# Optimization experiments

Hardware: AMD Instinct MI355X
Metric: run time of the kernel (lower is better)

Reference implementation:

```python
import jax, jax.numpy as jnp
import numpy as np

NUM_HEADS = 16


def rotate_half(x):
    half = x.shape[-1] // 2
    return jnp.concatenate((-x[..., half:], x[..., :half]), axis=-1)


def rope_tables(seq_len, head_dim, dtype=jnp.float32):
    inv_freq = 1.0 / (10000.0 ** (jnp.arange(0, head_dim, 2, dtype=jnp.float32) / head_dim))
    t = jnp.arange(seq_len, dtype=jnp.float32)
    freqs = jnp.outer(t, inv_freq)                 # [S, hd/2]
    emb = jnp.concatenate((freqs, freqs), axis=-1)  # [S, hd]
    return jnp.cos(emb).astype(dtype), jnp.sin(emb).astype(dtype)


def setup_inputs() -> dict:
    key = jax.random.key(0)
    k1, k2, k3 = jax.random.split(key, 3)
    B, S, D = 2, 2048, 1024
    x = jax.random.normal(k1, (B, S, D), dtype=jnp.float32)
    # causal lower-triangular mask, broadcast over batch/heads
    mask = jnp.tril(jnp.ones((S, S), dtype=bool))[None, None, :, :]
    w_qkv = jax.random.normal(k2, (3 * D, D), dtype=jnp.float32) * (D ** -0.5)
    w_out = jax.random.normal(k3, (D, D), dtype=jnp.float32) * (D ** -0.5)
    return {"x": x, "mask": mask, "w_qkv": w_qkv, "w_out": w_out}


def reference(x, mask, w_qkv, w_out):
    B, S, D = x.shape
    H = NUM_HEADS
    hd = D // H
    scale = hd ** -0.5

    qkv = jnp.einsum('bsd,ed->bse', x, w_qkv)          # [B, S, 3D]
    q, k, v = jnp.split(qkv, 3, axis=-1)

    def split(t):
        return t.reshape(B, S, H, hd).transpose(0, 2, 1, 3)  # [B, H, S, hd]

    q, k, v = split(q), split(k), split(v)

    cos, sin = rope_tables(S, hd, x.dtype)             # [S, hd]
    cos = cos[None, None]
    sin = sin[None, None]
    q = q * cos + rotate_half(q) * sin
    k = k * cos + rotate_half(k) * sin

    attn = jnp.einsum('bhqd,bhkd->bhqk', q, k) * scale  # [B, H, S, S]
    attn = jnp.where(mask, attn, jnp.float32(-jnp.inf).astype(attn.dtype))
    attn = jax.nn.softmax(attn, axis=-1)
    out = jnp.einsum('bhqk,bhkd->bhqd', attn, v)        # [B, H, S, hd]
    out = out.transpose(0, 2, 1, 3).reshape(B, S, D)
    return jnp.einsum('bsd,ed->bse', out, w_out)
```

## Files before the change

### kernel.cpp

```cpp
#include <hip/hip_runtime.h>
#include <hip/hip_bf16.h>

typedef __attribute__((ext_vector_type(8))) __bf16 bf16x8;
typedef __attribute__((ext_vector_type(4))) __bf16 bf16x4;
typedef __attribute__((ext_vector_type(2))) __bf16 bf16x2;
typedef __attribute__((ext_vector_type(4))) float f32x4;
typedef __attribute__((ext_vector_type(16))) float f32x16;

#define SEQ 2048
#define NH 16
#define HD 64
#define DMODEL 1024
#define BATCH 2
#define MTOT 4096
#define NSLOT 72

#if __has_builtin(__builtin_amdgcn_exp2f)
#define EXP2(x) __builtin_amdgcn_exp2f(x)
#else
#define EXP2(x) exp2f(x)
#endif
#define MFMA32(a, b, c) __builtin_amdgcn_mfma_f32_32x32x16_bf16(a, b, c, 0, 0, 0)

__device__ __forceinline__ void gl_lds16(const void* g, void* l) {
    __builtin_amdgcn_global_load_lds(
        (const __attribute__((address_space(1))) void*)(uintptr_t)g,
        (__attribute__((address_space(3))) void*)(uintptr_t)l,
        16, 0, 0);
}

__device__ __forceinline__ unsigned pk2(float x, float y) {
    union { bf16x2 h; unsigned u; } c;
    c.h = bf16x2{ (__bf16)x, (__bf16)y };
    return c.u;
}

#define TILE_SYNC(N) do {                                           \
    asm volatile("s_waitcnt vmcnt(" #N ")" ::: "memory");           \
    __builtin_amdgcn_s_barrier();                                   \
    __builtin_amdgcn_sched_barrier(0);                              \
} while (0)

__constant__ int4 FITEM[80] = {
    {31,0,16,68},{31,16,32,69},{31,32,48,70},{31,48,64,71},
    {23,0,16,37},{23,16,32,38},{23,32,48,39},
    {15,0,16,14},{15,16,32,15},
    {30,15,31,65},{30,46,62,67},
    {22,30,46,36},
    {7,0,16,-1},
    {29,0,15,60},{29,15,30,61},{29,30,45,62},{29,45,60,63},
    {30,0,15,64},{30,31,46,66},
    {22,0,15,34},{22,15,30,35},
    {21,14,29,32},{21,29,44,33},
    {28,14,29,57},{28,43,58,59},
    {14,0,15,12},{14,15,30,13},
    {27,0,14,52},{27,14,28,53},{27,28,42,54},{27,42,56,55},
    {28,0,14,56},{28,29,43,58},
    {20,0,14,28},{20,14,28,29},{20,28,42,30},
    {21,0,14,31},
    {26,13,27,49},{26,40,54,51},
    {19,26,40,27},
    {13,0,14,10},{13,14,28,11},
    {6,0,14,-1},
    {25,0,13,44},{25,13,26,45},{25,26,39,46},{25,39,52,47},
    {26,0,13,48},{26,27,40,50},
    {24,12,25,41},{24,37,50,43},
    {19,0,13,25},{19,13,26,26},
    {18,12,25,23},{18,25,38,24},
    {12,0,13,8},{12,13,26,9},
    {24,0,12,40},{24,25,37,42},
    {17,0,12,19},{17,12,24,20},{17,24,36,21},
    {18,0,12,22},
    {16,22,34,18},
    {11,0,12,6},{11,12,24,7},
    {5,0,12,-1},
    {16,0,11,16},{16,11,22,17},
    {10,0,11,4},{10,11,22,5},
    {9,0,10,2},{9,10,20,3},
    {4,0,10,-1},
    {8,0,9,0},{8,9,18,1},
    {3,0,8,-1},{2,0,6,-1},{1,0,4,-1},{0,0,2,-1}
};

__global__ __launch_bounds__(256) void cast3(const float4* __restrict__ x,
                                             const float4* __restrict__ wq,
                                             const float4* __restrict__ wo,
                                             __bf16* __restrict__ xb,
                                             __bf16* __restrict__ wqb,
                                             __bf16* __restrict__ wob) {
    const int NX  = 1024 * 1024;
    const int NWQ = 768 * 1024;
    const int NTOT = NX + NWQ + 256 * 1024;
    int i = blockIdx.x * 256 + threadIdx.x;
    if (i >= NTOT) return;
    float4 v; __bf16* dst; int j;
    if (i < NX)            { j = i;            v = x[j];  dst = xb;  }
    else if (i < NX + NWQ) { j = i - NX;       v = wq[j]; dst = wqb; }
    else                   { j = i - NX - NWQ; v = wo[j]; dst = wob; }
    bf16x4 o = { (__bf16)v.x, (__bf16)v.y, (__bf16)v.z, (__bf16)v.w };
    *(bf16x4*)(dst + (size_t)j * 4) = o;
}

__global__ __launch_bounds__(256) void gemm_qkv(const __bf16* __restrict__ A,
                                                const __bf16* __restrict__ Bt,
                                                __bf16* __restrict__ Qp,
                                                char* __restrict__ K2,
                                                char* __restrict__ V2) {
    const int K = 1024;
    __shared__ __align__(16) char lds[3 * 16384];
    const int tid = threadIdx.x, lane = tid & 63, wave = tid >> 6;
    const int lrow = lane & 15, quad = lane >> 4;
    const int bx = blockIdx.x, by = blockIdx.y;
    const int m0 = by * 128, n0 = bx * 128;
    const int wm = wave >> 1, wn = wave & 1;

    const __bf16* ap[2]; int aof[2];
    const __bf16* bp[2]; int bof[2];
#pragma unroll
    for (int i = 0; i < 2; ++i) {
        int r0 = i * 64 + wave * 16;
        int row = r0 + (lane >> 2);
        ap[i] = A + (size_t)(m0 + row) * K + (lane & 3) * 8;
        aof[i] = r0 * 64;
        bp[i] = Bt + (size_t)(n0 + row) * K + (lane & 3) * 8;
        bof[i] = 8192 + r0 * 64;
    }
    int arow[4], brow[4];
#pragma unroll
    for (int i = 0; i < 4; ++i) {
        arow[i] = wm * 64 + i * 16 + lrow;
        brow[i] = wn * 64 + i * 16 + lrow;
    }

    f32x4 z = {0.f, 0.f, 0.f, 0.f};
    f32x4 acc[4][4];
#pragma unroll
    for (int i = 0; i < 4; ++i)
#pragma unroll
        for (int j = 0; j < 4; ++j) acc[i][j] = z;

    auto STAGE = [&](char* base, int k0) {
#pragma unroll
        for (int i = 0; i < 2; ++i) gl_lds16(ap[i] + k0, base + aof[i]);
#pragma unroll
        for (int i = 0; i < 2; ++i) gl_lds16(bp[i] + k0, base + bof[i]);
    };
    auto COMPUTE = [&](const char* base) {
        bf16x8 af[4], bfr[4];
#pragma unroll
        for (int i = 0; i < 4; ++i)
            af[i] = *(const bf16x8*)(base + arow[i] * 64 + quad * 16);
#pragma unroll
        for (int i = 0; i < 4; ++i)
            bfr[i] = *(const bf16x8*)(base + 8192 + brow[i] * 64 + quad * 16);
        __builtin_amdgcn_s_setprio(1);
#pragma unroll
        for (int i = 0; i < 4; ++i)
#pragma unroll
            for (int j = 0; j < 4; ++j)
                acc[i][j] = __builtin_amdgcn_mfma_f32_16x16x32_bf16(
                    af[i], bfr[j], acc[i][j], 0, 0, 0);
        __builtin_amdgcn_s_setprio(0);
    };

    STAGE(lds, 0);
    STAGE(lds + 16384, 32);
    TILE_SYNC(4);
    for (int t = 0; t < 30; ++t) {
        STAGE(lds + ((t + 2) % 3) * 16384, (t + 2) * 32);
        COMPUTE(lds + (t % 3) * 16384);
        TILE_SYNC(4);
    }
    COMPUTE(lds + 0 * 16384);
    TILE_SYNC(0);
    COMPUTE(lds + 1 * 16384);

    const int nt = bx;
    const int sec = nt >> 3;
    const int b = m0 >> 11;
    const int s0b = m0 & (SEQ - 1);
    const int h = (nt & 7) * 2 + wn;
    const int bh = b * NH + h;

    if (sec < 2) {
        const float scale = sec ? 1.0f : 0.18033688011112042f;
        char* Kb = K2 + (size_t)bh * 262144;
        float invf0 = 0.15915494309189535f *
                      exp2f(-(float)lrow * 0.4152410118609203f);
        float invf1 = invf0 * 0.01f;
#pragma unroll
        for (int i = 0; i < 4; ++i) {
            int srow0 = s0b + wm * 64 + i * 16 + quad * 4;
#pragma unroll
            for (int j = 0; j < 2; ++j) {
                float invf = j ? invf1 : invf0;
                int hdlo = j * 16 + lrow;
#pragma unroll
                for (int r = 0; r < 4; ++r) {
                    int s = srow0 + r;
                    float rev = (float)s * invf;
                    float fr = rev - floorf(rev);
                    float sn = __builtin_amdgcn_sinf(fr);
                    float cs = __builtin_amdgcn_cosf(fr);
                    float lo = acc[i][j][r], hi = acc[i][j + 2][r];
                    float olo = (lo * cs - hi * sn) * scale;
                    float ohi = (hi * cs + lo * sn) * scale;
                    if (sec == 0) {
                        size_t base = ((size_t)bh * SEQ + s) * HD + hdlo;
                        Qp[base] = (__bf16)olo;
                        Qp[base + 32] = (__bf16)ohi;
                    } else {
                        char* kt = Kb + (s >> 5) * 4096 + (s & 31) * 16 +
                                   ((lrow >> 3) & 1) * 512 + (lrow & 7) * 2;
                        *(__bf16*)(kt + j * 1024) = (__bf16)olo;
                        *(__bf16*)(kt + (j + 2) * 1024) = (__bf16)ohi;
                    }
                }
            }
        }
    } else {
        char* Vb = V2 + (size_t)bh * 262144;
#pragma unroll
        for (int i = 0; i < 4; ++i) {
            int srow0 = s0b + wm * 64 + i * 16 + quad * 4;
            int kb = srow0 >> 4, ko = srow0 & 15;
            int slot0 = ((ko >> 2) & 1) * 8 + (ko >> 3) * 4;
#pragma unroll
            for (int j = 0; j < 4; ++j) {
                int ch = j * 16 + lrow;
                bf16x4 wv = { (__bf16)acc[i][j][0], (__bf16)acc[i][j][1],
                              (__bf16)acc[i][j][2], (__bf16)acc[i][j][3] };
                *(bf16x4*)(Vb + kb * 2048 + ch * 32 + slot0 * 2) = wv;
            }
        }
    }
}

__global__ __launch_bounds__(256) void gemm_bt(const __bf16* __restrict__ A,
                                               const __bf16* __restrict__ Bt,
                                               float* __restrict__ Cf,
                                               int M, int N, int K) {
    __shared__ __bf16 sA[2][128 * 64];
    __shared__ __bf16 sB[2][128 * 64];
    const int tid = threadIdx.x, lane = tid & 63, wave = tid >> 6;
    const int lrow = lane & 15, quad = lane >> 4;

    int lin = blockIdx.y * 8 + blockIdx.x;
    lin = (lin & 7) * 32 + (lin >> 3);
    const int bx = lin & 7, by = lin >> 3;
    const int m0 = by * 128, n0 = bx * 128;
    const int wm = wave >> 1, wn = wave & 1;

    const __bf16* ap[4]; const __bf16* bp[4]; int ldso[4];
#pragma unroll
    for (int i = 0; i < 4; ++i) {
        int r0 = i * 32 + wave * 8;
        int row = r0 + (lane >> 3);
        int cg = (lane & 7) ^ (row & 7);
        ap[i] = A + (size_t)(m0 + row) * K + cg * 8;
        bp[i] = Bt + (size_t)(n0 + row) * K + cg * 8;
        ldso[i] = r0 * 128;
    }
    int arow[4], brow[4];
#pragma unroll
    for (int i = 0; i < 4; ++i) {
        arow[i] = wm * 64 + i * 16 + lrow;
        brow[i] = wn * 64 + i * 16 + lrow;
    }

    f32x4 z = {0.f, 0.f, 0.f, 0.f};
    f32x4 acc[4][4];
#pragma unroll
    for (int i = 0; i < 4; ++i)
#pragma unroll
        for (int j = 0; j < 4; ++j) acc[i][j] = z;

    char* sA0 = (char*)sA[0]; char* sA1 = (char*)sA[1];
    char* sB0 = (char*)sB[0]; char* sB1 = (char*)sB[1];

    auto STAGE = [&](char* dA, char* dB, int k0) {
#pragma unroll
        for (int i = 0; i < 4; ++i) gl_lds16(ap[i] + k0, dA + ldso[i]);
#pragma unroll
        for (int i = 0; i < 4; ++i) gl_lds16(bp[i] + k0, dB + ldso[i]);
    };
    auto COMPUTE = [&](const char* sAb, const char* sBb) {
#pragma unroll
        for (int ks = 0; ks < 2; ++ks) {
            bf16x8 af[4], bfr[4];
#pragma unroll
            for (int i = 0; i < 4; ++i)
                af[i] = *(const bf16x8*)(sAb + arow[i] * 128 +
                                         (((ks * 4 + quad) ^ (arow[i] & 7)) << 4));
#pragma unroll
            for (int i = 0; i < 4; ++i)
                bfr[i] = *(const bf16x8*)(sBb + brow[i] * 128 +
                                          (((ks * 4 + quad) ^ (brow[i] & 7)) << 4));
#pragma unroll
            for (int i = 0; i < 4; ++i)
#pragma unroll
                for (int j = 0; j < 4; ++j)
                    acc[i][j] = __builtin_amdgcn_mfma_f32_16x16x32_bf16(
                        af[i], bfr[j], acc[i][j], 0, 0, 0);
        }
    };

    STAGE(sA0, sB0, 0);
    __syncthreads();
    for (int k0 = 0; k0 < K; k0 += 128) {
        if (k0 + 64 < K) STAGE(sA1, sB1, k0 + 64);
        COMPUTE(sA0, sB0);
        __syncthreads();
        if (k0 + 128 < K) STAGE(sA0, sB0, k0 + 128);
        COMPUTE(sA1, sB1);
        __syncthreads();
    }
#pragma unroll
    for (int i = 0; i < 4; ++i)
#pragma unroll
        for (int j = 0; j < 4; ++j)
#pragma unroll
            for (int r = 0; r < 4; ++r) {
                int row = m0 + wm * 64 + i * 16 + quad * 4 + r;
                int col = n0 + wn * 64 + j * 16 + lrow;
                Cf[(size_t)row * N + col] = acc[i][j][r];
            }
}

__global__ __launch_bounds__(64) void flash_attn(const __bf16* __restrict__ Qp,
                                                 const char* __restrict__ K2,
                                                 const char* __restrict__ V2,
                                                 __bf16* __restrict__ Aout,
                                                 __bf16* __restrict__ Opart,
                                                 float* __restrict__ Lpart) {
    const int lane = threadIdx.x;
    const int ql = lane & 31, half = lane >> 5;
    const int lin = blockIdx.x;
    const int xcd = lin & 7;
    const int j = lin >> 3;
    const int item = j % 80;
    const int bgroup = j / 80;
    const int bh = bgroup * 8 + xcd;
    const int4 it = FITEM[item];
    const int s = it.x, t0 = it.y, t1 = it.z, slot = it.w;
    const int b = bh >> 4, hh = bh & 15;

    const __bf16* qb = Qp + ((size_t)bh * SEQ + s * 64 + ql) * HD + half * 8;
    bf16x8 qf0[4], qf1[4];
#pragma unroll
    for (int kc = 0; kc < 4; ++kc) {
        qf0[kc] = *(const bf16x8*)(qb + kc * 16);
        qf1[kc] = *(const bf16x8*)(qb + 32 * HD + kc * 16);
    }
    const char* Kb = K2 + (size_t)bh * 262144 + half * 512 + ql * 16;
    const char* Vb = V2 + (size_t)bh * 262144 + ql * 32 + half * 16;

    f32x16 zz = {0.f};
    f32x16 oA0 = zz, oA1 = zz, oB0 = zz, oB1 = zz;
    float lA = 0.f, lB = 0.f;
    const int dA = 2 * s, dB = 2 * s + 1;
    const int thr = ql - 4 * half;

    auto STEP = [&](int t, const bf16x8* kf, bf16x8* kn) {
        bf16x8 vf[2][2];
#pragma unroll
        for (int lo = 0; lo < 2; ++lo) {
            const char* vp = Vb + (t * 2 + lo) * 2048;
            vf[lo][0] = *(const bf16x8*)(vp);
            vf[lo][1] = *(const bf16x8*)(vp + 1024);
        }
        if (t + 1 < t1) {
            const char* kt = Kb + (t + 1) * 4096;
#pragma unroll
            for (int kc = 0; kc < 4; ++kc)
                kn[kc] = *(const bf16x8*)(kt + kc * 1024);
        }
        const bool do0 = (t != dB);
        f32x16 st0 = zz, st1 = zz;
        if (do0) {
#pragma unroll
            for (int kc = 0; kc < 4; ++kc)
                st0 = MFMA32(kf[kc], qf0[kc], st0);
        }
#pragma unroll
        for (int kc = 0; kc < 4; ++kc)
            st1 = MFMA32(kf[kc], qf1[kc], st1);

        if (do0) {
#pragma unroll
            for (int i = 0; i < 16; ++i) st0[i] = EXP2(st0[i]);
            if (t == dA) {
#pragma unroll
                for (int g = 0; g < 4; ++g)
#pragma unroll
                    for (int tt = 0; tt < 4; ++tt)
                        if (8 * g + tt > thr) st0[g * 4 + tt] = 0.f;
            }
#pragma unroll
            for (int i = 0; i < 16; ++i) lA += st0[i];
        }
#pragma unroll
        for (int i = 0; i < 16; ++i) st1[i] = EXP2(st1[i]);
        if (t == dB) {
#pragma unroll
            for (int g = 0; g < 4; ++g)
#pragma unroll
                for (int tt = 0; tt < 4; ++tt)
                    if (8 * g + tt > thr) st1[g * 4 + tt] = 0.f;
        }
#pragma unroll
        for (int i = 0; i < 16; ++i) lB += st1[i];

#pragma unroll
        for (int lo = 0; lo < 2; ++lo) {
            if (do0) {
                union { unsigned u[4]; bf16x8 v; } p0;
#pragma unroll
                for (int d = 0; d < 4; ++d)
                    p0.u[d] = pk2(st0[lo * 8 + 2 * d], st0[lo * 8 + 2 * d + 1]);
                oA0 = MFMA32(vf[lo][0], p0.v, oA0);
                oA1 = MFMA32(vf[lo][1], p0.v, oA1);
            }
            union { unsigned u[4]; bf16x8 v; } p1;
#pragma unroll
            for (int d = 0; d < 4; ++d)
                p1.u[d] = pk2(st1[lo * 8 + 2 * d], st1[lo * 8 + 2 * d + 1]);
            oB0 = MFMA32(vf[lo][0], p1.v, oB0);
            oB1 = MFMA32(vf[lo][1], p1.v, oB1);
        }
    };

    bf16x8 kA[4], kB[4];
    {
        const char* kt = Kb + t0 * 4096;
#pragma unroll
        for (int kc = 0; kc < 4; ++kc)
            kA[kc] = *(const bf16x8*)(kt + kc * 1024);
    }
    int t = t0;
    while (true) {
        STEP(t, kA, kB);
        if (++t >= t1) break;
        STEP(t, kB, kA);
        if (++t >= t1) break;
    }

    lA += __shfl_xor(lA, 32, 64);
    lB += __shfl_xor(lB, 32, 64);

    if (slot < 0) {
        float iA = 1.0f / lA, iB = 1.0f / lB;
        __bf16* oa = Aout + ((size_t)b * SEQ + s * 64 + ql) * DMODEL + hh * HD;
        __bf16* ob = oa + (size_t)32 * DMODEL;
#pragma unroll
        for (int g = 0; g < 4; ++g) {
            bf16x4 wA0 = { (__bf16)(oA0[g*4+0]*iA), (__bf16)(oA0[g*4+1]*iA),
                           (__bf16)(oA0[g*4+2]*iA), (__bf16)(oA0[g*4+3]*iA) };
            bf16x4 wA1 = { (__bf16)(oA1[g*4+0]*iA), (__bf16)(oA1[g*4+1]*iA),
                           (__bf16)(oA1[g*4+2]*iA), (__bf16)(oA1[g*4+3]*iA) };
            bf16x4 wB0 = { (__bf16)(oB0[g*4+0]*iB), (__bf16)(oB0[g*4+1]*iB),
                           (__bf16)(oB0[g*4+2]*iB), (__bf16)(oB0[g*4+3]*iB) };
            bf16x4 wB1 = { (__bf16)(oB1[g*4+0]*iB), (__bf16)(oB1[g*4+1]*iB),
                           (__bf16)(oB1[g*4+2]*iB), (__bf16)(oB1[g*4+3]*iB) };
            *(bf16x4*)(oa + 8 * g + 4 * half) = wA0;
            *(bf16x4*)(oa + 32 + 8 * g + 4 * half) = wA1;
            *(bf16x4*)(ob + 8 * g + 4 * half) = wB0;
            *(bf16x4*)(ob + 32 + 8 * g + 4 * half) = wB1;
        }
    } else {
        __bf16* oa = Opart + ((size_t)(bh * NSLOT + slot) << 12) + ql * 64;
        __bf16* ob = oa + 32 * 64;
#pragma unroll
        for (int g = 0; g < 4; ++g) {
            bf16x4 wA0 = { (__bf16)oA0[g*4+0], (__bf16)oA0[g*4+1],
                           (__bf16)oA0[g*4+2], (__bf16)oA0[g*4+3] };
            bf16x4 wA1 = { (__bf16)oA1[g*4+0], (__bf16)oA1[g*4+1],
                           (__bf16)oA1[g*4+2], (__bf16)oA1[g*4+3] };
            bf16x4 wB0 = { (__bf16)oB0[g*4+0], (__bf16)oB0[g*4+1],
                           (__bf16)oB0[g*4+2], (__bf16)oB0[g*4+3] };
            bf16x4 wB1 = { (__bf16)oB1[g*4+0], (__bf16)oB1[g*4+1],
                           (__bf16)oB1[g*4+2], (__bf16)oB1[g*4+3] };
            *(bf16x4*)(oa + 8 * g + 4 * half) = wA0;
            *(bf16x4*)(oa + 32 + 8 * g + 4 * half) = wA1;
            *(bf16x4*)(ob + 8 * g + 4 * half) = wB0;
            *(bf16x4*)(ob + 32 + 8 * g + 4 * half) = wB1;
        }
        if (!half) {
            Lpart[(bh * NSLOT + slot) * 64 + ql] = lA;
            Lpart[(bh * NSLOT + slot) * 64 + 32 + ql] = lB;
        }
    }
}

__global__ __launch_bounds__(256) void combine(const __bf16* __restrict__ Opart,
                                               const float* __restrict__ Lpart,
                                               __bf16* __restrict__ Aout) {
    const int bh = blockIdx.x;
    const int s = 8 + blockIdx.y;
    const int C = (s < 16) ? 2 : ((s < 24) ? 3 : 4);
    const int base = (s < 16) ? (s - 8) * 2
                   : (s < 24) ? 16 + (s - 16) * 3
                              : 40 + (s - 24) * 4;
    const int t = threadIdx.x;
    const int r = t >> 2, cg = (t & 3) * 16;
    float acc[16];
#pragma unroll
    for (int i = 0; i < 16; ++i) acc[i] = 0.f;
    float l = 0.f;
    for (int ci = 0; ci < C; ++ci) {
        int ch = bh * NSLOT + base + ci;
        l += Lpart[ch * 64 + r];
        const __bf16* p = Opart + ((size_t)ch << 12) + r * 64 + cg;
#pragma unroll
        for (int k = 0; k < 2; ++k) {
            bf16x8 v = ((const bf16x8*)p)[k];
#pragma unroll
            for (int j = 0; j < 8; ++j) acc[k * 8 + j] += (float)v[j];
        }
    }
    float invl = 1.0f / l;
    const int b = bh >> 4, hh = bh & 15;
    __bf16* dst = Aout + ((size_t)(b * SEQ + s * 64 + r)) * DMODEL +
                  hh * 64 + cg;
#pragma unroll
    for (int k = 0; k < 2; ++k) {
        bf16x8 w;
#pragma unroll
        for (int j = 0; j < 8; ++j) w[j] = (__bf16)(acc[k * 8 + j] * invl);
        ((bf16x8*)dst)[k] = w;
    }
}

extern "C" void kernel_launch(void* const* d_in, const int* in_sizes, int n_in,
                              void* d_out, int out_size, void* d_ws, size_t ws_size,
                              hipStream_t stream) {
    (void)in_sizes; (void)n_in; (void)out_size; (void)ws_size;
    const float* x  = (const float*)d_in[0];
    const float* wq = (const float*)d_in[2];
    const float* wo = (const float*)d_in[3];
    float* out = (float*)d_out;

    char* w = (char*)d_ws;
    __bf16* xb   = (__bf16*)(w);
    __bf16* wqb  = (__bf16*)(w + (8ull << 20));
    __bf16* wob  = (__bf16*)(w + (14ull << 20));
    __bf16* Opart= (__bf16*)(w + (16ull << 20));
    float*  Lpart= (float*) (w + (35ull << 20));
    __bf16* Qb   = (__bf16*)(w + (40ull << 20));
    char*   K2   = (char*)  (w + (48ull << 20));
    char*   V2   = (char*)  (w + (56ull << 20));
    __bf16* aob  = xb;

    cast3<<<8192, 256, 0, stream>>>((const float4*)x, (const float4*)wq,
                                    (const float4*)wo, xb, wqb, wob);
    gemm_qkv<<<dim3(24, 32), 256, 0, stream>>>(xb, wqb, Qb, K2, V2);
    flash_attn<<<2560, 64, 0, stream>>>(Qb, K2, V2, aob, Opart, Lpart);
    combine<<<dim3(32, 24), 256, 0, stream>>>(Opart, Lpart, aob);
    gemm_bt<<<dim3(8, 32), 256, 0, stream>>>(aob, wob, out, MTOT, 1024, 1024);
}
```

Measured before the change: 187.7 us.

## Triple-buffer output GEMM with K=32 tiles and pack attention items into 4-wave blocks

The output projection GEMM moves from a double-buffered K=64 LDS pipeline with full barriers to a triple-buffered K=32 ring. It uses vmcnt-based waits and raises wave priority around the MFMA block, so global loads overlap more with compute. The flash attention kernel now launches 4-wave blocks, each running four work items from a reordered item table grouped by similar length. That cuts the launch count and balances the waves inside a block. Risks are LDS bank conflicts, because the XOR swizzle is dropped in the GEMM, and idle waves inside a block when the grouped items differ in length.

```diff
diff --git a/kernel.cpp b/kernel.cpp
--- a/kernel.cpp
+++ b/kernel.cpp
@@ -42,43 +42,25 @@
 } while (0)
 
 __constant__ int4 FITEM[80] = {
-    {31,0,16,68},{31,16,32,69},{31,32,48,70},{31,48,64,71},
-    {23,0,16,37},{23,16,32,38},{23,32,48,39},
-    {15,0,16,14},{15,16,32,15},
-    {30,15,31,65},{30,46,62,67},
-    {22,30,46,36},
-    {7,0,16,-1},
-    {29,0,15,60},{29,15,30,61},{29,30,45,62},{29,45,60,63},
-    {30,0,15,64},{30,31,46,66},
-    {22,0,15,34},{22,15,30,35},
-    {21,14,29,32},{21,29,44,33},
-    {28,14,29,57},{28,43,58,59},
-    {14,0,15,12},{14,15,30,13},
-    {27,0,14,52},{27,14,28,53},{27,28,42,54},{27,42,56,55},
-    {28,0,14,56},{28,29,43,58},
-    {20,0,14,28},{20,14,28,29},{20,28,42,30},
-    {21,0,14,31},
-    {26,13,27,49},{26,40,54,51},
-    {19,26,40,27},
-    {13,0,14,10},{13,14,28,11},
-    {6,0,14,-1},
-    {25,0,13,44},{25,13,26,45},{25,26,39,46},{25,39,52,47},
-    {26,0,13,48},{26,27,40,50},
-    {24,12,25,41},{24,37,50,43},
-    {19,0,13,25},{19,13,26,26},
-    {18,12,25,23},{18,25,38,24},
-    {12,0,13,8},{12,13,26,9},
-    {24,0,12,40},{24,25,37,42},
-    {17,0,12,19},{17,12,24,20},{17,24,36,21},
-    {18,0,12,22},
-    {16,22,34,18},
-    {11,0,12,6},{11,12,24,7},
-    {5,0,12,-1},
-    {16,0,11,16},{16,11,22,17},
-    {10,0,11,4},{10,11,22,5},
-    {9,0,10,2},{9,10,20,3},
-    {4,0,10,-1},
-    {8,0,9,0},{8,9,18,1},
+    {31,0,16,68},{23,0,16,37},{15,0,16,14},{7,0,16,-1},
+    {31,16,32,69},{23,16,32,38},{15,16,32,15},{30,15,31,65},
+    {31,32,48,70},{23,32,48,39},{30,31,46,66},{29,30,45,62},
+    {31,48,64,71},{30,46,62,67},{29,45,60,63},{28,43,58,59},
+    {22,30,46,36},{18,25,38,24},{17,24,36,21},{16,22,34,18},
+    {30,0,15,64},{29,0,15,60},{22,0,15,34},{14,0,15,12},
+    {29,15,30,61},{22,15,30,35},{14,15,30,13},{28,14,29,57},
+    {27,14,28,53},{20,14,28,29},{13,14,28,11},{21,14,29,32},
+    {27,28,42,54},{20,28,42,30},{28,29,43,58},{21,29,44,33},
+    {28,0,14,56},{27,0,14,52},{21,0,14,31},{20,0,14,28},
+    {13,0,14,10},{6,0,14,-1},{25,0,13,44},{26,0,13,48},
+    {26,13,27,49},{25,13,26,45},{19,13,26,26},{12,13,26,9},
+    {26,27,40,50},{25,26,39,46},{19,26,40,27},{24,25,37,42},
+    {26,40,54,51},{25,39,52,47},{24,37,50,43},{27,42,56,55},
+    {19,0,13,25},{12,0,13,8},{5,0,12,-1},{18,0,12,22},
+    {24,12,25,41},{18,12,25,23},{17,12,24,20},{11,12,24,7},
+    {24,0,12,40},{17,0,12,19},{11,0,12,6},{16,0,11,16},
+    {16,11,22,17},{10,11,22,5},{9,10,20,3},{8,9,18,1},
+    {10,0,11,4},{9,0,10,2},{8,0,9,0},{4,0,10,-1},
     {3,0,8,-1},{2,0,6,-1},{1,0,4,-1},{0,0,2,-1}
 };
 
@@ -240,8 +222,7 @@
                                                const __bf16* __restrict__ Bt,
                                                float* __restrict__ Cf,
                                                int M, int N, int K) {
-    __shared__ __bf16 sA[2][128 * 64];
-    __shared__ __bf16 sB[2][128 * 64];
+    __shared__ __align__(16) char lds[3 * 16384];
     const int tid = threadIdx.x, lane = tid & 63, wave = tid >> 6;
     const int lrow = lane & 15, quad = lane >> 4;
 
@@ -251,15 +232,16 @@
     const int m0 = by * 128, n0 = bx * 128;
     const int wm = wave >> 1, wn = wave & 1;
 
-    const __bf16* ap[4]; const __bf16* bp[4]; int ldso[4];
-#pragma unroll
-    for (int i = 0; i < 4; ++i) {
-        int r0 = i * 32 + wave * 8;
-        int row = r0 + (lane >> 3);
-        int cg = (lane & 7) ^ (row & 7);
-        ap[i] = A + (size_t)(m0 + row) * K + cg * 8;
-        bp[i] = Bt + (size_t)(n0 + row) * K + cg * 8;
-        ldso[i] = r0 * 128;
+    const __bf16* ap[2]; int aof[2];
+    const __bf16* bp[2]; int bof[2];
+#pragma unroll
+    for (int i = 0; i < 2; ++i) {
+        int r0 = i * 64 + wave * 16;
+        int row = r0 + (lane >> 2);
+        ap[i] = A + (size_t)(m0 + row) * K + (lane & 3) * 8;
+        aof[i] = r0 * 64;
+        bp[i] = Bt + (size_t)(n0 + row) * K + (lane & 3) * 8;
+        bof[i] = 8192 + r0 * 64;
     }
     int arow[4], brow[4];
 #pragma unroll
@@ -275,46 +257,43 @@
 #pragma unroll
         for (int j = 0; j < 4; ++j) acc[i][j] = z;
 
-    char* sA0 = (char*)sA[0]; char* sA1 = (char*)sA[1];
-    char* sB0 = (char*)sB[0]; char* sB1 = (char*)sB[1];
-
-    auto STAGE = [&](char* dA, char* dB, int k0) {
-#pragma unroll
-        for (int i = 0; i < 4; ++i) gl_lds16(ap[i] + k0, dA + ldso[i]);
-#pragma unroll
-        for (int i = 0; i < 4; ++i) gl_lds16(bp[i] + k0, dB + ldso[i]);
+    auto STAGE = [&](char* base, int k0) {
+#pragma unroll
+        for (int i = 0; i < 2; ++i) gl_lds16(ap[i] + k0, base + aof[i]);
+#pragma unroll
+        for (int i = 0; i < 2; ++i) gl_lds16(bp[i] + k0, base + bof[i]);
     };
-    auto COMPUTE = [&](const char* sAb, const char* sBb) {
-#pragma unroll
-        for (int ks = 0; ks < 2; ++ks) {
-            bf16x8 af[4], bfr[4];
-#pragma unroll
-            for (int i = 0; i < 4; ++i)
-                af[i] = *(const bf16x8*)(sAb + arow[i] * 128 +
-                                         (((ks * 4 + quad) ^ (arow[i] & 7)) << 4));
-#pragma unroll
-            for (int i = 0; i < 4; ++i)
-                bfr[i] = *(const bf16x8*)(sBb + brow[i] * 128 +
-                                          (((ks * 4 + quad) ^ (brow[i] & 7)) << 4));
-#pragma unroll
-            for (int i = 0; i < 4; ++i)
-#pragma unroll
-                for (int j = 0; j < 4; ++j)
-                    acc[i][j] = __builtin_amdgcn_mfma_f32_16x16x32_bf16(
-                        af[i], bfr[j], acc[i][j], 0, 0, 0);
-        }
+    auto COMPUTE = [&](const char* base) {
+        bf16x8 af[4], bfr[4];
+#pragma unroll
+        for (int i = 0; i < 4; ++i)
+            af[i] = *(const bf16x8*)(base + arow[i] * 64 + quad * 16);
+#pragma unroll
+        for (int i = 0; i < 4; ++i)
+            bfr[i] = *(const bf16x8*)(base + 8192 + brow[i] * 64 + quad * 16);
+        __builtin_amdgcn_s_setprio(1);
+#pragma unroll
+        for (int i = 0; i < 4; ++i)
+#pragma unroll
+            for (int j = 0; j < 4; ++j)
+                acc[i][j] = __builtin_amdgcn_mfma_f32_16x16x32_bf16(
+                    af[i], bfr[j], acc[i][j], 0, 0, 0);
+        __builtin_amdgcn_s_setprio(0);
     };
 
-    STAGE(sA0, sB0, 0);
-    __syncthreads();
-    for (int k0 = 0; k0 < K; k0 += 128) {
-        if (k0 + 64 < K) STAGE(sA1, sB1, k0 + 64);
-        COMPUTE(sA0, sB0);
-        __syncthreads();
-        if (k0 + 128 < K) STAGE(sA0, sB0, k0 + 128);
-        COMPUTE(sA1, sB1);
-        __syncthreads();
-    }
+    const int ntk = K >> 5;
+    STAGE(lds, 0);
+    STAGE(lds + 16384, 32);
+    TILE_SYNC(4);
+    for (int t = 0; t + 2 < ntk; ++t) {
+        STAGE(lds + ((t + 2) % 3) * 16384, (t + 2) * 32);
+        COMPUTE(lds + (t % 3) * 16384);
+        TILE_SYNC(4);
+    }
+    COMPUTE(lds + ((ntk - 2) % 3) * 16384);
+    TILE_SYNC(0);
+    COMPUTE(lds + ((ntk - 1) % 3) * 16384);
+
 #pragma unroll
     for (int i = 0; i < 4; ++i)
 #pragma unroll
@@ -327,21 +306,22 @@
             }
 }
 
-__global__ __launch_bounds__(64) void flash_attn(const __bf16* __restrict__ Qp,
-                                                 const char* __restrict__ K2,
-                                                 const char* __restrict__ V2,
-                                                 __bf16* __restrict__ Aout,
-                                                 __bf16* __restrict__ Opart,
-                                                 float* __restrict__ Lpart) {
-    const int lane = threadIdx.x;
+__global__ __launch_bounds__(256) void flash_attn(const __bf16* __restrict__ Qp,
+                                                  const char* __restrict__ K2,
+                                                  const char* __restrict__ V2,
+                                                  __bf16* __restrict__ Aout,
+                                                  __bf16* __restrict__ Opart,
+                                                  float* __restrict__ Lpart) {
+    const int lane = threadIdx.x & 63;
+    const int wave = threadIdx.x >> 6;
     const int ql = lane & 31, half = lane >> 5;
     const int lin = blockIdx.x;
     const int xcd = lin & 7;
     const int j = lin >> 3;
-    const int item = j % 80;
-    const int bgroup = j / 80;
+    const int group = j % 20;
+    const int bgroup = j / 20;
     const int bh = bgroup * 8 + xcd;
-    const int4 it = FITEM[item];
+    const int4 it = FITEM[group * 4 + wave];
     const int s = it.x, t0 = it.y, t1 = it.z, slot = it.w;
     const int b = bh >> 4, hh = bh & 15;
 
@@ -554,7 +534,7 @@
     cast3<<<8192, 256, 0, stream>>>((const float4*)x, (const float4*)wq,
                                     (const float4*)wo, xb, wqb, wob);
     gemm_qkv<<<dim3(24, 32), 256, 0, stream>>>(xb, wqb, Qb, K2, V2);
-    flash_attn<<<2560, 64, 0, stream>>>(Qb, K2, V2, aob, Opart, Lpart);
+    flash_attn<<<640, 256, 0, stream>>>(Qb, K2, V2, aob, Opart, Lpart);
     combine<<<dim3(32, 24), 256, 0, stream>>>(Opart, Lpart, aob);
     gemm_bt<<<dim3(8, 32), 256, 0, stream>>>(aob, wob, out, MTOT, 1024, 1024);
 }
```

After: 194.5 us. +3.6%, slower.
